# Kernel optimization log

Measured on AMD Instinct MI355X. Metric: run time of the kernel, lower is better.

Reference implementation:

```python
import jax, jax.numpy as jnp
import numpy as np

N = 100000       # nodes
E = 3200000      # edges (avg degree 32)
IN = 64          # in_channels
HID = 32         # hidden_channels
HEADS = 2
OUT = 1
EPS = 1e-5       # LayerNorm eps
SLOPE = 0.2      # LeakyReLU negative slope (PyG default)


def setup_inputs() -> dict:
    key = jax.random.key(0)
    ks = jax.random.split(key, 18)
    def nrm(k, shape, scale=0.1):
        return jax.random.normal(k, shape, dtype=jnp.float32) * scale
    return {
        "x": jax.random.normal(ks[0], (N, IN), dtype=jnp.float32),
        "edge_index": jax.random.randint(ks[1], (2, E), 0, N, dtype=jnp.int64),
        # GATConv layer 1 (concat=True)
        "W1": nrm(ks[2], (IN, HEADS * HID)),
        "a_src1": nrm(ks[3], (HEADS, HID)),
        "a_dst1": nrm(ks[4], (HEADS, HID)),
        "b1": jnp.zeros((HEADS * HID,), jnp.float32),
        "ln1_g": jnp.ones((HEADS * HID,), jnp.float32),
        "ln1_b": jnp.zeros((HEADS * HID,), jnp.float32),
        # GATConv layer 2 (heads=1, concat=False)
        "W2": nrm(ks[5], (HEADS * HID, HID)),
        "a_src2": nrm(ks[6], (1, HID)),
        "a_dst2": nrm(ks[7], (1, HID)),
        "b2": jnp.zeros((HID,), jnp.float32),
        "ln2_g": jnp.ones((HID,), jnp.float32),
        "ln2_b": jnp.zeros((HID,), jnp.float32),
        # output Linear
        "Wout": nrm(ks[8], (HID, OUT)),
        "bout": jnp.zeros((OUT,), jnp.float32),
    }


def layer_norm(x, g, b):
    mu = jnp.mean(x, axis=-1, keepdims=True)
    var = jnp.mean(jnp.square(x - mu), axis=-1, keepdims=True)
    return (x - mu) * jax.lax.rsqrt(var + EPS) * g + b


def gat_conv(x, edge_index, W, a_src, a_dst, bias, heads, ch, concat):
    """PyG GATConv (add_self_loops=True, bias=True), eval mode (no dropout)."""
    n = x.shape[0]
    loop = jnp.arange(n, dtype=edge_index.dtype)
    src = jnp.concatenate([edge_index[0], loop])   # [E+N]
    dst = jnp.concatenate([edge_index[1], loop])   # [E+N]
    h = (x @ W).reshape(n, heads, ch)              # [N,H,C]
    al_src = jnp.sum(h * a_src, axis=-1)           # [N,H]
    al_dst = jnp.sum(h * a_dst, axis=-1)           # [N,H]
    logits = jax.nn.leaky_relu(al_src[src] + al_dst[dst], SLOPE)  # [E+N,H]
    # segment softmax over destination nodes
    m = jax.lax.stop_gradient(jax.ops.segment_max(logits, dst, num_segments=n))
    e = jnp.exp(logits - m[dst])
    denom = jax.ops.segment_sum(e, dst, num_segments=n)
    alpha = e / denom[dst]                         # [E+N,H]
    out = jax.ops.segment_sum(h[src] * alpha[:, :, None], dst, num_segments=n)  # [N,H,C]
    out = out.reshape(n, heads * ch) if concat else out.mean(axis=1)
    return out + bias


def reference(x, edge_index, W1, a_src1, a_dst1, b1, ln1_g, ln1_b,
              W2, a_src2, a_dst2, b2, ln2_g, ln2_b, Wout, bout):
    h = gat_conv(x, edge_index, W1, a_src1, a_dst1, b1, HEADS, HID, True)
    h = jax.nn.elu(layer_norm(h, ln1_g, ln1_b))
    h = gat_conv(h, edge_index, W2, a_src2, a_dst2, b2, 1, HID, False)
    h = jax.nn.elu(layer_norm(h, ln2_g, ln2_b))
    return h @ Wout + bout  # [N, OUT]
```

## Files before the change

### kernel.cpp

```cpp
#include <hip/hip_runtime.h>

#define EPS 1e-5f
#define SLOPE 0.2f
#define MAXK 512
#define SEGCAP 12288
#define PBATCH 8192

__device__ __forceinline__ float leaky(float z) {
    return fmaxf(z, 0.f) + SLOPE * fminf(z, 0.f);
}
__device__ __forceinline__ ushort f2bf(float f) {
    unsigned u = __float_as_uint(f);
    u += 0x7FFFu + ((u >> 16) & 1u);
    return (ushort)(u >> 16);
}
__device__ __forceinline__ float bf2f(ushort b) {
    return __uint_as_float(((unsigned)b) << 16);
}

__global__ __launch_bounds__(1024) void part1(
    const int* __restrict__ ei, int E, int K, int* __restrict__ segcnt,
    unsigned* __restrict__ part) {
    __shared__ int h[MAXK];
    __shared__ int gp[MAXK];
    __shared__ int run[MAXK];
    int t = threadIdx.x;
    for (int i = t; i < K; i += 1024) { h[i] = 0; run[i] = 0; }
    __syncthreads();
    int base = blockIdx.x * PBATCH;
    int sv[PBATCH / 1024], dv[PBATCH / 1024];
#pragma unroll
    for (int j = 0; j < PBATCH / 1024; j++) {
        int e = base + j * 1024 + t;
        sv[j] = (e < E) ? ei[e] : -1;
        dv[j] = (e < E) ? ei[E + e] : -1;
        if (dv[j] >= 0) atomicAdd(&h[dv[j] >> 8], 1);
    }
    __syncthreads();
    for (int i = t; i < K; i += 1024)
        gp[i] = h[i] ? atomicAdd(&segcnt[i * 16], h[i]) : 0;
    __syncthreads();
#pragma unroll
    for (int j = 0; j < PBATCH / 1024; j++) {
        if (dv[j] >= 0) {
            int b = dv[j] >> 8;
            int p = atomicAdd(&run[b], 1) + gp[b];
            if (p < SEGCAP)
                part[(size_t)b * SEGCAP + p] =
                    ((unsigned)sv[j] << 8) | (unsigned)(dv[j] & 255);
        }
    }
}

__global__ __launch_bounds__(256) void sortseg(
    const int* __restrict__ segcnt, int N,
    unsigned* __restrict__ part, int* __restrict__ nodeofs, int* __restrict__ cnt,
    int* __restrict__ perm) {
    __shared__ int h2[4096];
    __shared__ int sc[256];
    __shared__ int ex[256];
    __shared__ unsigned outb[SEGCAP];
    int b = blockIdx.x, t = threadIdx.x;
    size_t base = (size_t)b * SEGCAP;
    int sz = min(segcnt[b * 16], SEGCAP);
    for (int i = t; i < 4096; i += 256) h2[i] = 0;
    __syncthreads();
    for (int i = t; i < sz; i += 256) {
        unsigned code = part[base + i];
        int key = ((code & 255) << 4) | ((code >> 21) & 15);
        atomicAdd(&h2[key], 1);
    }
    __syncthreads();
    int loc[16];
    int v = 0;
#pragma unroll
    for (int i = 0; i < 16; i++) { loc[i] = h2[t * 16 + i]; v += loc[i]; }
    sc[t] = v;
    __syncthreads();
    for (int off = 1; off < 256; off <<= 1) {
        int x = (t >= off) ? sc[t - off] : 0;
        __syncthreads();
        sc[t] += x;
        __syncthreads();
    }
    int exv = sc[t] - v;
    {
        int run = exv;
#pragma unroll
        for (int i = 0; i < 16; i++) { h2[t * 16 + i] = run; run += loc[i]; }
    }
    int n = b * 256 + t;
    if (n < N) { cnt[n] = v; nodeofs[n] = (int)(base + exv); }
    __syncthreads();
    for (int i = t; i < sz; i += 256) {
        unsigned code = part[base + i];
        int key = ((code & 255) << 4) | ((code >> 21) & 15);
        int p = atomicAdd(&h2[key], 1);
        outb[p] = code >> 8;
    }
    __syncthreads();
    for (int i = t; i < sz; i += 256) part[base + i] = outb[i];
    __syncthreads();
    h2[t] = 0;
    __syncthreads();
    int dbin = min(v, 255);
    if (n < N) atomicAdd(&h2[dbin], 1);
    __syncthreads();
    int hv = h2[t];
    sc[t] = hv;
    __syncthreads();
    for (int off = 1; off < 256; off <<= 1) {
        int x = (t >= off) ? sc[t - off] : 0;
        __syncthreads();
        sc[t] += x;
        __syncthreads();
    }
    ex[t] = sc[t] - hv;
    __syncthreads();
    if (n < N) {
        int r = atomicAdd(&ex[dbin], 1);
        perm[b * 256 + r] = n;
    }
}

__global__ __launch_bounds__(256) void prep1(
    const float* __restrict__ x, const float* __restrict__ W1,
    const float* __restrict__ as1, const float* __restrict__ ad1,
    ushort* __restrict__ h1b, float* __restrict__ al_s, float* __restrict__ al_d, int N) {
    __shared__ float Ws[64 * 64];
    __shared__ float xs[16][68];
    int t = threadIdx.x;
    for (int i = t; i < 64 * 64; i += 256) Ws[i] = W1[i];
    int base = blockIdx.x * 16;
    for (int i = t; i < 256; i += 256) {
        int rr = i >> 4, kk = i & 15;
        int gr = base + rr;
        float4 vx = (gr < N) ? ((const float4*)x)[(size_t)gr * 16 + kk]
                             : make_float4(0.f, 0.f, 0.f, 0.f);
        *(float4*)&xs[rr][kk * 4] = vx;
    }
    __syncthreads();
    int wv = t >> 6, c = t & 63;
    int r0 = base + wv * 4;
    float acc0 = 0.f, acc1 = 0.f, acc2 = 0.f, acc3 = 0.f;
#pragma unroll
    for (int k = 0; k < 64; k += 4) {
        float4 x0 = *(const float4*)&xs[wv * 4 + 0][k];
        float4 x1 = *(const float4*)&xs[wv * 4 + 1][k];
        float4 x2 = *(const float4*)&xs[wv * 4 + 2][k];
        float4 x3 = *(const float4*)&xs[wv * 4 + 3][k];
        float w0 = Ws[(k + 0) * 64 + c];
        float w1 = Ws[(k + 1) * 64 + c];
        float w2 = Ws[(k + 2) * 64 + c];
        float w3 = Ws[(k + 3) * 64 + c];
        acc0 = fmaf(x0.x, w0, acc0); acc1 = fmaf(x1.x, w0, acc1);
        acc2 = fmaf(x2.x, w0, acc2); acc3 = fmaf(x3.x, w0, acc3);
        acc0 = fmaf(x0.y, w1, acc0); acc1 = fmaf(x1.y, w1, acc1);
        acc2 = fmaf(x2.y, w1, acc2); acc3 = fmaf(x3.y, w1, acc3);
        acc0 = fmaf(x0.z, w2, acc0); acc1 = fmaf(x1.z, w2, acc1);
        acc2 = fmaf(x2.z, w2, acc2); acc3 = fmaf(x3.z, w2, acc3);
        acc0 = fmaf(x0.w, w3, acc0); acc1 = fmaf(x1.w, w3, acc1);
        acc2 = fmaf(x2.w, w3, acc2); acc3 = fmaf(x3.w, w3, acc3);
    }
    int head = c >> 5, cc = c & 31;
    float asc = as1[head * 32 + cc], adc = ad1[head * 32 + cc];
    float vs0 = acc0 * asc, vd0 = acc0 * adc;
    float vs1 = acc1 * asc, vd1 = acc1 * adc;
    float vs2 = acc2 * asc, vd2 = acc2 * adc;
    float vs3 = acc3 * asc, vd3 = acc3 * adc;
#pragma unroll
    for (int off = 1; off < 32; off <<= 1) {
        vs0 += __shfl_xor(vs0, off); vd0 += __shfl_xor(vd0, off);
        vs1 += __shfl_xor(vs1, off); vd1 += __shfl_xor(vd1, off);
        vs2 += __shfl_xor(vs2, off); vd2 += __shfl_xor(vd2, off);
        vs3 += __shfl_xor(vs3, off); vd3 += __shfl_xor(vd3, off);
    }
    if (r0 + 0 < N) h1b[(size_t)(r0 + 0) * 64 + c] = f2bf(acc0);
    if (r0 + 1 < N) h1b[(size_t)(r0 + 1) * 64 + c] = f2bf(acc1);
    if (r0 + 2 < N) h1b[(size_t)(r0 + 2) * 64 + c] = f2bf(acc2);
    if (r0 + 3 < N) h1b[(size_t)(r0 + 3) * 64 + c] = f2bf(acc3);
    if (cc == 0) {
        if (r0 + 0 < N) { al_s[(r0 + 0) * 2 + head] = vs0; al_d[(r0 + 0) * 2 + head] = vd0; }
        if (r0 + 1 < N) { al_s[(r0 + 1) * 2 + head] = vs1; al_d[(r0 + 1) * 2 + head] = vd1; }
        if (r0 + 2 < N) { al_s[(r0 + 2) * 2 + head] = vs2; al_d[(r0 + 2) * 2 + head] = vd2; }
        if (r0 + 3 < N) { al_s[(r0 + 3) * 2 + head] = vs3; al_d[(r0 + 3) * 2 + head] = vd3; }
    }
}

__global__ __launch_bounds__(256) void aggB1(
    const ushort* __restrict__ h1b, const float* __restrict__ als,
    const float* __restrict__ ald, const int* __restrict__ nodeofs,
    const int* __restrict__ cnt, const unsigned* __restrict__ csr,
    const int* __restrict__ perm,
    const float* __restrict__ b1, const float* __restrict__ g1,
    const float* __restrict__ bb1, ushort* __restrict__ h1out, int N) {
    int lane = threadIdx.x & 63;
    int grp = lane >> 4, q = lane & 15;
    int gbase = grp << 4;
    int idx = blockIdx.x * 16 + (threadIdx.x >> 6) * 4 + grp;
    bool valid = idx < N;
    int nc = perm[min(idx, N - 1)];
    int head = q >> 3;
    const float2* als2 = (const float2*)als;
    const float2* ald2 = (const float2*)ald;
    float2 adv = ald2[nc], asv = als2[nc];
    float ad0 = adv.x, ad1v = adv.y;
    float wsf = __expf(leaky((head ? asv.y : asv.x) + (head ? ad1v : ad0)));
    const ushort4* h4 = (const ushort4*)h1b;
    ushort4 hs = h4[(unsigned)nc * 16 + q];
    float a0 = wsf * bf2f(hs.x), a1 = wsf * bf2f(hs.y);
    float a2 = wsf * bf2f(hs.z), a3 = wsf * bf2f(hs.w);
    float l0p = 0.f, l1p = 0.f;
    int ofs = valid ? nodeofs[nc] : 0;
    int deg = valid ? cnt[nc] : 0;
    int degm1 = max(deg - 1, 0);
    int degmax = deg;
    degmax = max(degmax, __shfl_xor(degmax, 16));
    degmax = max(degmax, __shfl_xor(degmax, 32));
    for (int eb = 0; eb < degmax; eb += 16) {
        int j = ofs + min(eb + q, degm1);
        int sq = min((int)csr[j], N - 1);
        float2 av = als2[sq];
        float z0 = leaky(av.x + ad0);
        float z1 = leaky(av.y + ad1v);
        bool ev = (eb + q < deg);
        float w0q = ev ? __expf(z0) : 0.f;
        float w1q = ev ? __expf(z1) : 0.f;
        l0p += w0q;
        l1p += w1q;
#pragma unroll
        for (int jj = 0; jj < 16; jj++) {
            int s = __shfl(sq, gbase + jj);
            float w0 = __shfl(w0q, gbase + jj);
            float w1 = __shfl(w1q, gbase + jj);
            float w = head ? w1 : w0;
            ushort4 hv = h4[(unsigned)s * 16 + q];
            a0 = fmaf(w, bf2f(hv.x), a0);
            a1 = fmaf(w, bf2f(hv.y), a1);
            a2 = fmaf(w, bf2f(hv.z), a2);
            a3 = fmaf(w, bf2f(hv.w), a3);
        }
    }
#pragma unroll
    for (int off = 1; off < 16; off <<= 1) {
        l0p += __shfl_xor(l0p, off);
        l1p += __shfl_xor(l1p, off);
    }
    if (!valid) return;
    float l = (head ? l1p : l0p) + wsf;
    float inv = 1.f / l;
    float4 bv = ((const float4*)b1)[q];
    float v0 = a0 * inv + bv.x, v1 = a1 * inv + bv.y;
    float v2 = a2 * inv + bv.z, v3 = a3 * inv + bv.w;
    float s1 = v0 + v1 + v2 + v3;
#pragma unroll
    for (int off = 1; off < 16; off <<= 1) s1 += __shfl_xor(s1, off);
    float mu = s1 * (1.f / 64.f);
    float d0 = v0 - mu, d1 = v1 - mu, d2 = v2 - mu, d3 = v3 - mu;
    float s2v = d0 * d0 + d1 * d1 + d2 * d2 + d3 * d3;
#pragma unroll
    for (int off = 1; off < 16; off <<= 1) s2v += __shfl_xor(s2v, off);
    float rs = rsqrtf(s2v * (1.f / 64.f) + EPS);
    float4 gv = ((const float4*)g1)[q];
    float4 bbv = ((const float4*)bb1)[q];
    float y0 = d0 * rs * gv.x + bbv.x;
    float y1 = d1 * rs * gv.y + bbv.y;
    float y2 = d2 * rs * gv.z + bbv.z;
    float y3 = d3 * rs * gv.w + bbv.w;
    y0 = (y0 > 0.f) ? y0 : (__expf(y0) - 1.f);
    y1 = (y1 > 0.f) ? y1 : (__expf(y1) - 1.f);
    y2 = (y2 > 0.f) ? y2 : (__expf(y2) - 1.f);
    y3 = (y3 > 0.f) ? y3 : (__expf(y3) - 1.f);
    ((ushort4*)h1out)[(unsigned)nc * 16 + q] =
        make_ushort4(f2bf(y0), f2bf(y1), f2bf(y2), f2bf(y3));
}

__global__ __launch_bounds__(256) void prep2(
    const ushort* __restrict__ h1ob, const float* __restrict__ W2,
    const float* __restrict__ as2, const float* __restrict__ ad2,
    ushort* __restrict__ h2b, float* __restrict__ al_s, float* __restrict__ al_d, int N) {
    __shared__ float Ws[64 * 32];
    __shared__ float xs[32][68];
    int t = threadIdx.x;
    for (int i = t; i < 64 * 32; i += 256) Ws[i] = W2[i];
    int base = blockIdx.x * 32;
    const ushort4* hv4 = (const ushort4*)h1ob;
    for (int i = t; i < 512; i += 256) {
        int rr = i >> 4, kk = i & 15;
        int gr = base + rr;
        ushort4 u = (gr < N) ? hv4[(unsigned)gr * 16 + kk] : make_ushort4(0, 0, 0, 0);
        xs[rr][kk * 4 + 0] = bf2f(u.x);
        xs[rr][kk * 4 + 1] = bf2f(u.y);
        xs[rr][kk * 4 + 2] = bf2f(u.z);
        xs[rr][kk * 4 + 3] = bf2f(u.w);
    }
    __syncthreads();
    int wv = t >> 6;
    int lane = t & 63;
    int half = lane >> 5, c = lane & 31;
    int rbase = wv * 8 + half * 4;
    int r0 = base + rbase;
    float acc0 = 0.f, acc1 = 0.f, acc2 = 0.f, acc3 = 0.f;
#pragma unroll
    for (int k = 0; k < 64; k += 4) {
        float4 x0 = *(const float4*)&xs[rbase + 0][k];
        float4 x1 = *(const float4*)&xs[rbase + 1][k];
        float4 x2 = *(const float4*)&xs[rbase + 2][k];
        float4 x3 = *(const float4*)&xs[rbase + 3][k];
        float w0 = Ws[(k + 0) * 32 + c];
        float w1 = Ws[(k + 1) * 32 + c];
        float w2 = Ws[(k + 2) * 32 + c];
        float w3 = Ws[(k + 3) * 32 + c];
        acc0 = fmaf(x0.x, w0, acc0); acc1 = fmaf(x1.x, w0, acc1);
        acc2 = fmaf(x2.x, w0, acc2); acc3 = fmaf(x3.x, w0, acc3);
        acc0 = fmaf(x0.y, w1, acc0); acc1 = fmaf(x1.y, w1, acc1);
        acc2 = fmaf(x2.y, w1, acc2); acc3 = fmaf(x3.y, w1, acc3);
        acc0 = fmaf(x0.z, w2, acc0); acc1 = fmaf(x1.z, w2, acc1);
        acc2 = fmaf(x2.z, w2, acc2); acc3 = fmaf(x3.z, w2, acc3);
        acc0 = fmaf(x0.w, w3, acc0); acc1 = fmaf(x1.w, w3, acc1);
        acc2 = fmaf(x2.w, w3, acc2); acc3 = fmaf(x3.w, w3, acc3);
    }
    float asc = as2[c], adc = ad2[c];
    float vs0 = acc0 * asc, vd0 = acc0 * adc;
    float vs1 = acc1 * asc, vd1 = acc1 * adc;
    float vs2 = acc2 * asc, vd2 = acc2 * adc;
    float vs3 = acc3 * asc, vd3 = acc3 * adc;
#pragma unroll
    for (int off = 1; off < 32; off <<= 1) {
        vs0 += __shfl_xor(vs0, off); vd0 += __shfl_xor(vd0, off);
        vs1 += __shfl_xor(vs1, off); vd1 += __shfl_xor(vd1, off);
        vs2 += __shfl_xor(vs2, off); vd2 += __shfl_xor(vd2, off);
        vs3 += __shfl_xor(vs3, off); vd3 += __shfl_xor(vd3, off);
    }
    if (r0 + 0 < N) h2b[(size_t)(r0 + 0) * 32 + c] = f2bf(acc0);
    if (r0 + 1 < N) h2b[(size_t)(r0 + 1) * 32 + c] = f2bf(acc1);
    if (r0 + 2 < N) h2b[(size_t)(r0 + 2) * 32 + c] = f2bf(acc2);
    if (r0 + 3 < N) h2b[(size_t)(r0 + 3) * 32 + c] = f2bf(acc3);
    if (c == 0) {
        if (r0 + 0 < N) { al_s[r0 + 0] = vs0; al_d[r0 + 0] = vd0; }
        if (r0 + 1 < N) { al_s[r0 + 1] = vs1; al_d[r0 + 1] = vd1; }
        if (r0 + 2 < N) { al_s[r0 + 2] = vs2; al_d[r0 + 2] = vd2; }
        if (r0 + 3 < N) { al_s[r0 + 3] = vs3; al_d[r0 + 3] = vd3; }
    }
}

__global__ __launch_bounds__(256) void aggB2(
    const ushort* __restrict__ h2b, const float* __restrict__ als,
    const float* __restrict__ ald, const int* __restrict__ nodeofs,
    const int* __restrict__ cnt, const unsigned* __restrict__ csr,
    const int* __restrict__ perm,
    const float* __restrict__ b2, const float* __restrict__ g2,
    const float* __restrict__ bb2, const float* __restrict__ Wout,
    const float* __restrict__ bout, float* __restrict__ out, int N) {
    int lane = threadIdx.x & 63;
    int grp = lane >> 3, q = lane & 7;
    int gbase = grp << 3;
    int idx = blockIdx.x * 32 + (threadIdx.x >> 6) * 8 + grp;
    bool valid = idx < N;
    int nc = perm[min(idx, N - 1)];
    float myad = ald[nc];
    float wsf = __expf(leaky(als[nc] + myad));
    const ushort4* h4 = (const ushort4*)h2b;
    ushort4 hs = h4[(unsigned)nc * 8 + q];
    float a0 = wsf * bf2f(hs.x), a1 = wsf * bf2f(hs.y);
    float a2 = wsf * bf2f(hs.z), a3 = wsf * bf2f(hs.w);
    float lp = 0.f;
    int ofs = valid ? nodeofs[nc] : 0;
    int deg = valid ? cnt[nc] : 0;
    int degm1 = max(deg - 1, 0);
    int degmax = deg;
    degmax = max(degmax, __shfl_xor(degmax, 8));
    degmax = max(degmax, __shfl_xor(degmax, 16));
    degmax = max(degmax, __shfl_xor(degmax, 32));
    for (int eb = 0; eb < degmax; eb += 8) {
        int j = ofs + min(eb + q, degm1);
        int sq = min((int)csr[j], N - 1);
        float z = leaky(als[sq] + myad);
        float wq = (eb + q < deg) ? __expf(z) : 0.f;
        lp += wq;
#pragma unroll
        for (int jj = 0; jj < 8; jj++) {
            int s = __shfl(sq, gbase + jj);
            float w = __shfl(wq, gbase + jj);
            ushort4 hv = h4[(unsigned)s * 8 + q];
            a0 = fmaf(w, bf2f(hv.x), a0);
            a1 = fmaf(w, bf2f(hv.y), a1);
            a2 = fmaf(w, bf2f(hv.z), a2);
            a3 = fmaf(w, bf2f(hv.w), a3);
        }
    }
#pragma unroll
    for (int off = 1; off < 8; off <<= 1) lp += __shfl_xor(lp, off);
    if (!valid) return;
    float l = lp + wsf;
    float inv = 1.f / l;
    float4 bv = ((const float4*)b2)[q];
    float v0 = a0 * inv + bv.x, v1 = a1 * inv + bv.y;
    float v2 = a2 * inv + bv.z, v3 = a3 * inv + bv.w;
    float s1 = v0 + v1 + v2 + v3;
#pragma unroll
    for (int off = 1; off < 8; off <<= 1) s1 += __shfl_xor(s1, off);
    float mu = s1 * (1.f / 32.f);
    float d0 = v0 - mu, d1 = v1 - mu, d2 = v2 - mu, d3 = v3 - mu;
    float s2v = d0 * d0 + d1 * d1 + d2 * d2 + d3 * d3;
#pragma unroll
    for (int off = 1; off < 8; off <<= 1) s2v += __shfl_xor(s2v, off);
    float rs = rsqrtf(s2v * (1.f / 32.f) + EPS);
    float4 gv = ((const float4*)g2)[q];
    float4 bbv = ((const float4*)bb2)[q];
    float y0 = d0 * rs * gv.x + bbv.x;
    float y1 = d1 * rs * gv.y + bbv.y;
    float y2 = d2 * rs * gv.z + bbv.z;
    float y3 = d3 * rs * gv.w + bbv.w;
    y0 = (y0 > 0.f) ? y0 : (__expf(y0) - 1.f);
    y1 = (y1 > 0.f) ? y1 : (__expf(y1) - 1.f);
    y2 = (y2 > 0.f) ? y2 : (__expf(y2) - 1.f);
    y3 = (y3 > 0.f) ? y3 : (__expf(y3) - 1.f);
    float4 wo = ((const float4*)Wout)[q];
    float p = y0 * wo.x + y1 * wo.y + y2 * wo.z + y3 * wo.w;
#pragma unroll
    for (int off = 1; off < 8; off <<= 1) p += __shfl_xor(p, off);
    if (q == 0) out[nc] = p + bout[0];
}

extern "C" void kernel_launch(void* const* d_in, const int* in_sizes, int n_in,
                              void* d_out, int out_size, void* d_ws, size_t ws_size,
                              hipStream_t stream) {
    const float* x    = (const float*)d_in[0];
    const int*   ei   = (const int*)d_in[1];
    const float* W1   = (const float*)d_in[2];
    const float* as1  = (const float*)d_in[3];
    const float* ad1  = (const float*)d_in[4];
    const float* b1   = (const float*)d_in[5];
    const float* g1   = (const float*)d_in[6];
    const float* bb1  = (const float*)d_in[7];
    const float* W2   = (const float*)d_in[8];
    const float* as2  = (const float*)d_in[9];
    const float* ad2  = (const float*)d_in[10];
    const float* b2   = (const float*)d_in[11];
    const float* g2   = (const float*)d_in[12];
    const float* bb2  = (const float*)d_in[13];
    const float* Wout = (const float*)d_in[14];
    const float* bout = (const float*)d_in[15];
    float* out = (float*)d_out;

    const int N = in_sizes[0] / 64;
    const int E = in_sizes[1] / 2;
    const int K = (N + 255) / 256;

    auto align_up = [](size_t v) { return (v + 255) & ~(size_t)255; };
    char* ws = (char*)d_ws;
    unsigned* part    = (unsigned*)ws; ws += align_up((size_t)K * SEGCAP * 4);
    int*      segcnt  = (int*)ws;      ws += align_up((size_t)MAXK * 16 * 4);
    int*      nodeofs = (int*)ws;      ws += align_up((size_t)N * 4);
    int*      cnt     = (int*)ws;      ws += align_up((size_t)N * 4);
    int*      perm    = (int*)ws;      ws += align_up((size_t)(K * 256) * 4);
    ushort*   h1b     = (ushort*)ws;   ws += align_up((size_t)N * 64 * 2);
    ushort*   h1ob    = (ushort*)ws;   ws += align_up((size_t)N * 64 * 2);
    ushort*   h2b     = (ushort*)ws;   ws += align_up((size_t)N * 32 * 2);
    float*    al1s    = (float*)ws;    ws += align_up((size_t)N * 2 * 4);
    float*    al1d    = (float*)ws;    ws += align_up((size_t)N * 2 * 4);
    float*    al2s    = (float*)ws;    ws += align_up((size_t)N * 4);
    float*    al2d    = (float*)ws;    ws += align_up((size_t)N * 4);

    const int EB = (E + PBATCH - 1) / PBATCH;

    hipMemsetAsync(segcnt, 0, (size_t)K * 16 * 4, stream);
    part1<<<EB, 1024, 0, stream>>>(ei, E, K, segcnt, part);
    sortseg<<<K, 256, 0, stream>>>(segcnt, N, part, nodeofs, cnt, perm);

    prep1<<<(N + 15) / 16, 256, 0, stream>>>(x, W1, as1, ad1, h1b, al1s, al1d, N);
    aggB1<<<(N + 15) / 16, 256, 0, stream>>>(h1b, al1s, al1d, nodeofs, cnt, part,
                                             perm, b1, g1, bb1, h1ob, N);
    prep2<<<(N + 31) / 32, 256, 0, stream>>>(h1ob, W2, as2, ad2, h2b, al2s, al2d, N);
    aggB2<<<(N + 31) / 32, 256, 0, stream>>>(h2b, al2s, al2d, nodeofs, cnt, part,
                                             perm, b2, g2, bb2, Wout, bout, out, N);
}
```

Before: 327.8 us.

## Fuse edge partition with layer-1 projection and layer-2 projection into aggregation

Merges the edge-partitioning kernel and the first linear projection into one launch, with block index selecting the role, so the projection runs alongside partitioning. Moves the second layer's linear projection and attention-logit computation into the first aggregation kernel using warp shuffles and W2 in shared memory. This removes the intermediate bf16 layer-1 output buffer round trip and two kernel launches. In exchange, the fused kernels use more shared memory and registers, and the 1024-thread projection blocks may lower occupancy.

Measured after the change: 319.8 us. 1.02x faster.

```diff
diff --git a/kernel.cpp b/kernel.cpp
--- a/kernel.cpp
+++ b/kernel.cpp
@@ -18,122 +18,52 @@
     return __uint_as_float(((unsigned)b) << 16);
 }
 
-__global__ __launch_bounds__(1024) void part1(
+__global__ __launch_bounds__(1024) void fused1(
     const int* __restrict__ ei, int E, int K, int* __restrict__ segcnt,
-    unsigned* __restrict__ part) {
-    __shared__ int h[MAXK];
-    __shared__ int gp[MAXK];
-    __shared__ int run[MAXK];
-    int t = threadIdx.x;
-    for (int i = t; i < K; i += 1024) { h[i] = 0; run[i] = 0; }
-    __syncthreads();
-    int base = blockIdx.x * PBATCH;
-    int sv[PBATCH / 1024], dv[PBATCH / 1024];
-#pragma unroll
-    for (int j = 0; j < PBATCH / 1024; j++) {
-        int e = base + j * 1024 + t;
-        sv[j] = (e < E) ? ei[e] : -1;
-        dv[j] = (e < E) ? ei[E + e] : -1;
-        if (dv[j] >= 0) atomicAdd(&h[dv[j] >> 8], 1);
-    }
-    __syncthreads();
-    for (int i = t; i < K; i += 1024)
-        gp[i] = h[i] ? atomicAdd(&segcnt[i * 16], h[i]) : 0;
-    __syncthreads();
-#pragma unroll
-    for (int j = 0; j < PBATCH / 1024; j++) {
-        if (dv[j] >= 0) {
-            int b = dv[j] >> 8;
-            int p = atomicAdd(&run[b], 1) + gp[b];
-            if (p < SEGCAP)
-                part[(size_t)b * SEGCAP + p] =
-                    ((unsigned)sv[j] << 8) | (unsigned)(dv[j] & 255);
-        }
-    }
-}
-
-__global__ __launch_bounds__(256) void sortseg(
-    const int* __restrict__ segcnt, int N,
-    unsigned* __restrict__ part, int* __restrict__ nodeofs, int* __restrict__ cnt,
-    int* __restrict__ perm) {
-    __shared__ int h2[4096];
-    __shared__ int sc[256];
-    __shared__ int ex[256];
-    __shared__ unsigned outb[SEGCAP];
-    int b = blockIdx.x, t = threadIdx.x;
-    size_t base = (size_t)b * SEGCAP;
-    int sz = min(segcnt[b * 16], SEGCAP);
-    for (int i = t; i < 4096; i += 256) h2[i] = 0;
-    __syncthreads();
-    for (int i = t; i < sz; i += 256) {
-        unsigned code = part[base + i];
-        int key = ((code & 255) << 4) | ((code >> 21) & 15);
-        atomicAdd(&h2[key], 1);
-    }
-    __syncthreads();
-    int loc[16];
-    int v = 0;
-#pragma unroll
-    for (int i = 0; i < 16; i++) { loc[i] = h2[t * 16 + i]; v += loc[i]; }
-    sc[t] = v;
-    __syncthreads();
-    for (int off = 1; off < 256; off <<= 1) {
-        int x = (t >= off) ? sc[t - off] : 0;
-        __syncthreads();
-        sc[t] += x;
-        __syncthreads();
-    }
-    int exv = sc[t] - v;
-    {
-        int run = exv;
-#pragma unroll
-        for (int i = 0; i < 16; i++) { h2[t * 16 + i] = run; run += loc[i]; }
-    }
-    int n = b * 256 + t;
-    if (n < N) { cnt[n] = v; nodeofs[n] = (int)(base + exv); }
-    __syncthreads();
-    for (int i = t; i < sz; i += 256) {
-        unsigned code = part[base + i];
-        int key = ((code & 255) << 4) | ((code >> 21) & 15);
-        int p = atomicAdd(&h2[key], 1);
-        outb[p] = code >> 8;
-    }
-    __syncthreads();
-    for (int i = t; i < sz; i += 256) part[base + i] = outb[i];
-    __syncthreads();
-    h2[t] = 0;
-    __syncthreads();
-    int dbin = min(v, 255);
-    if (n < N) atomicAdd(&h2[dbin], 1);
-    __syncthreads();
-    int hv = h2[t];
-    sc[t] = hv;
-    __syncthreads();
-    for (int off = 1; off < 256; off <<= 1) {
-        int x = (t >= off) ? sc[t - off] : 0;
-        __syncthreads();
-        sc[t] += x;
-        __syncthreads();
-    }
-    ex[t] = sc[t] - hv;
-    __syncthreads();
-    if (n < N) {
-        int r = atomicAdd(&ex[dbin], 1);
-        perm[b * 256 + r] = n;
-    }
-}
-
-__global__ __launch_bounds__(256) void prep1(
+    unsigned* __restrict__ part,
     const float* __restrict__ x, const float* __restrict__ W1,
     const float* __restrict__ as1, const float* __restrict__ ad1,
-    ushort* __restrict__ h1b, float* __restrict__ al_s, float* __restrict__ al_d, int N) {
-    __shared__ float Ws[64 * 64];
-    __shared__ float xs[16][68];
+    ushort* __restrict__ h1b, float* __restrict__ al_s, float* __restrict__ al_d,
+    int N, int EB) {
+    __shared__ float smem[4096 + 64 * 68];
     int t = threadIdx.x;
-    for (int i = t; i < 64 * 64; i += 256) Ws[i] = W1[i];
-    int base = blockIdx.x * 16;
-    for (int i = t; i < 256; i += 256) {
-        int rr = i >> 4, kk = i & 15;
+    if ((int)blockIdx.x < EB) {
+        int* h   = (int*)smem;
+        int* gp  = h + 512;
+        int* run = h + 1024;
+        for (int i = t; i < K; i += 1024) { h[i] = 0; run[i] = 0; }
+        __syncthreads();
+        int base = blockIdx.x * PBATCH;
+        int sv[PBATCH / 1024], dv[PBATCH / 1024];
+#pragma unroll
+        for (int j = 0; j < PBATCH / 1024; j++) {
+            int e = base + j * 1024 + t;
+            sv[j] = (e < E) ? ei[e] : -1;
+            dv[j] = (e < E) ? ei[E + e] : -1;
+            if (dv[j] >= 0) atomicAdd(&h[dv[j] >> 8], 1);
+        }
+        __syncthreads();
+        for (int i = t; i < K; i += 1024)
+            gp[i] = h[i] ? atomicAdd(&segcnt[i * 16], h[i]) : 0;
+        __syncthreads();
+#pragma unroll
+        for (int j = 0; j < PBATCH / 1024; j++) {
+            if (dv[j] >= 0) {
+                int b = dv[j] >> 8;
+                int p = atomicAdd(&run[b], 1) + gp[b];
+                if (p < SEGCAP)
+                    part[(size_t)b * SEGCAP + p] =
+                        ((unsigned)sv[j] << 8) | (unsigned)(dv[j] & 255);
+            }
+        }
+        return;
+    }
+    float* Ws = smem;
+    float (*xs)[68] = (float(*)[68])(smem + 4096);
+    for (int i = t; i < 4096; i += 1024) Ws[i] = W1[i];
+    int base = (blockIdx.x - EB) * 64;
+    {
+        int rr = t >> 4, kk = t & 15;
         int gr = base + rr;
         float4 vx = (gr < N) ? ((const float4*)x)[(size_t)gr * 16 + kk]
                              : make_float4(0.f, 0.f, 0.f, 0.f);
@@ -187,17 +117,96 @@
     }
 }
 
+__global__ __launch_bounds__(256) void sortseg(
+    const int* __restrict__ segcnt, int N,
+    unsigned* __restrict__ part, int* __restrict__ nodeofs, int* __restrict__ cnt,
+    int* __restrict__ perm) {
+    __shared__ int h2[4096];
+    __shared__ int sc[256];
+    __shared__ int ex[256];
+    __shared__ unsigned outb[SEGCAP];
+    int b = blockIdx.x, t = threadIdx.x;
+    size_t base = (size_t)b * SEGCAP;
+    int sz = min(segcnt[b * 16], SEGCAP);
+    for (int i = t; i < 4096; i += 256) h2[i] = 0;
+    __syncthreads();
+    for (int i = t; i < sz; i += 256) {
+        unsigned code = part[base + i];
+        int key = ((code & 255) << 4) | ((code >> 21) & 15);
+        atomicAdd(&h2[key], 1);
+    }
+    __syncthreads();
+    int loc[16];
+    int v = 0;
+#pragma unroll
+    for (int i = 0; i < 16; i++) { loc[i] = h2[t * 16 + i]; v += loc[i]; }
+    sc[t] = v;
+    __syncthreads();
+    for (int off = 1; off < 256; off <<= 1) {
+        int x = (t >= off) ? sc[t - off] : 0;
+        __syncthreads();
+        sc[t] += x;
+        __syncthreads();
+    }
+    int exv = sc[t] - v;
+    {
+        int run = exv;
+#pragma unroll
+        for (int i = 0; i < 16; i++) { h2[t * 16 + i] = run; run += loc[i]; }
+    }
+    int n = b * 256 + t;
+    if (n < N) { cnt[n] = v; nodeofs[n] = (int)(base + exv); }
+    __syncthreads();
+    for (int i = t; i < sz; i += 256) {
+        unsigned code = part[base + i];
+        int key = ((code & 255) << 4) | ((code >> 21) & 15);
+        int p = atomicAdd(&h2[key], 1);
+        outb[p] = code >> 8;
+    }
+    __syncthreads();
+    for (int i = t; i < sz; i += 256) part[base + i] = outb[i];
+    __syncthreads();
+    h2[t] = 0;
+    __syncthreads();
+    int dbin = min(v, 255);
+    if (n < N) atomicAdd(&h2[dbin], 1);
+    __syncthreads();
+    int hv = h2[t];
+    sc[t] = hv;
+    __syncthreads();
+    for (int off = 1; off < 256; off <<= 1) {
+        int x = (t >= off) ? sc[t - off] : 0;
+        __syncthreads();
+        sc[t] += x;
+        __syncthreads();
+    }
+    ex[t] = sc[t] - hv;
+    __syncthreads();
+    if (n < N) {
+        int r = atomicAdd(&ex[dbin], 1);
+        perm[b * 256 + r] = n;
+    }
+}
+
 __global__ __launch_bounds__(256) void aggB1(
     const ushort* __restrict__ h1b, const float* __restrict__ als,
     const float* __restrict__ ald, const int* __restrict__ nodeofs,
     const int* __restrict__ cnt, const unsigned* __restrict__ csr,
     const int* __restrict__ perm,
     const float* __restrict__ b1, const float* __restrict__ g1,
-    const float* __restrict__ bb1, ushort* __restrict__ h1out, int N) {
-    int lane = threadIdx.x & 63;
+    const float* __restrict__ bb1,
+    const float* __restrict__ W2, const float* __restrict__ as2,
+    const float* __restrict__ ad2,
+    ushort* __restrict__ h2b, float* __restrict__ al2s, float* __restrict__ al2d,
+    int N) {
+    __shared__ float W2s[64 * 32];
+    int t = threadIdx.x;
+    for (int i = t; i < 2048; i += 256) W2s[i] = W2[i];
+    __syncthreads();
+    int lane = t & 63;
     int grp = lane >> 4, q = lane & 15;
     int gbase = grp << 4;
-    int idx = blockIdx.x * 16 + (threadIdx.x >> 6) * 4 + grp;
+    int idx = blockIdx.x * 16 + (t >> 6) * 4 + grp;
     bool valid = idx < N;
     int nc = perm[min(idx, N - 1)];
     int head = q >> 3;
@@ -271,77 +280,36 @@
     y1 = (y1 > 0.f) ? y1 : (__expf(y1) - 1.f);
     y2 = (y2 > 0.f) ? y2 : (__expf(y2) - 1.f);
     y3 = (y3 > 0.f) ? y3 : (__expf(y3) - 1.f);
-    ((ushort4*)h1out)[(unsigned)nc * 16 + q] =
-        make_ushort4(f2bf(y0), f2bf(y1), f2bf(y2), f2bf(y3));
-}
-
-__global__ __launch_bounds__(256) void prep2(
-    const ushort* __restrict__ h1ob, const float* __restrict__ W2,
-    const float* __restrict__ as2, const float* __restrict__ ad2,
-    ushort* __restrict__ h2b, float* __restrict__ al_s, float* __restrict__ al_d, int N) {
-    __shared__ float Ws[64 * 32];
-    __shared__ float xs[32][68];
-    int t = threadIdx.x;
-    for (int i = t; i < 64 * 32; i += 256) Ws[i] = W2[i];
-    int base = blockIdx.x * 32;
-    const ushort4* hv4 = (const ushort4*)h1ob;
-    for (int i = t; i < 512; i += 256) {
-        int rr = i >> 4, kk = i & 15;
-        int gr = base + rr;
-        ushort4 u = (gr < N) ? hv4[(unsigned)gr * 16 + kk] : make_ushort4(0, 0, 0, 0);
-        xs[rr][kk * 4 + 0] = bf2f(u.x);
-        xs[rr][kk * 4 + 1] = bf2f(u.y);
-        xs[rr][kk * 4 + 2] = bf2f(u.z);
-        xs[rr][kk * 4 + 3] = bf2f(u.w);
-    }
-    __syncthreads();
-    int wv = t >> 6;
-    int lane = t & 63;
-    int half = lane >> 5, c = lane & 31;
-    int rbase = wv * 8 + half * 4;
-    int r0 = base + rbase;
-    float acc0 = 0.f, acc1 = 0.f, acc2 = 0.f, acc3 = 0.f;
-#pragma unroll
-    for (int k = 0; k < 64; k += 4) {
-        float4 x0 = *(const float4*)&xs[rbase + 0][k];
-        float4 x1 = *(const float4*)&xs[rbase + 1][k];
-        float4 x2 = *(const float4*)&xs[rbase + 2][k];
-        float4 x3 = *(const float4*)&xs[rbase + 3][k];
-        float w0 = Ws[(k + 0) * 32 + c];
-        float w1 = Ws[(k + 1) * 32 + c];
-        float w2 = Ws[(k + 2) * 32 + c];
-        float w3 = Ws[(k + 3) * 32 + c];
-        acc0 = fmaf(x0.x, w0, acc0); acc1 = fmaf(x1.x, w0, acc1);
-        acc2 = fmaf(x2.x, w0, acc2); acc3 = fmaf(x3.x, w0, acc3);
-        acc0 = fmaf(x0.y, w1, acc0); acc1 = fmaf(x1.y, w1, acc1);
-        acc2 = fmaf(x2.y, w1, acc2); acc3 = fmaf(x3.y, w1, acc3);
-        acc0 = fmaf(x0.z, w2, acc0); acc1 = fmaf(x1.z, w2, acc1);
-        acc2 = fmaf(x2.z, w2, acc2); acc3 = fmaf(x3.z, w2, acc3);
-        acc0 = fmaf(x0.w, w3, acc0); acc1 = fmaf(x1.w, w3, acc1);
-        acc2 = fmaf(x2.w, w3, acc2); acc3 = fmaf(x3.w, w3, acc3);
-    }
-    float asc = as2[c], adc = ad2[c];
-    float vs0 = acc0 * asc, vd0 = acc0 * adc;
-    float vs1 = acc1 * asc, vd1 = acc1 * adc;
-    float vs2 = acc2 * asc, vd2 = acc2 * adc;
-    float vs3 = acc3 * asc, vd3 = acc3 * adc;
-#pragma unroll
-    for (int off = 1; off < 32; off <<= 1) {
-        vs0 += __shfl_xor(vs0, off); vd0 += __shfl_xor(vd0, off);
-        vs1 += __shfl_xor(vs1, off); vd1 += __shfl_xor(vd1, off);
-        vs2 += __shfl_xor(vs2, off); vd2 += __shfl_xor(vd2, off);
-        vs3 += __shfl_xor(vs3, off); vd3 += __shfl_xor(vd3, off);
-    }
-    if (r0 + 0 < N) h2b[(size_t)(r0 + 0) * 32 + c] = f2bf(acc0);
-    if (r0 + 1 < N) h2b[(size_t)(r0 + 1) * 32 + c] = f2bf(acc1);
-    if (r0 + 2 < N) h2b[(size_t)(r0 + 2) * 32 + c] = f2bf(acc2);
-    if (r0 + 3 < N) h2b[(size_t)(r0 + 3) * 32 + c] = f2bf(acc3);
-    if (c == 0) {
-        if (r0 + 0 < N) { al_s[r0 + 0] = vs0; al_d[r0 + 0] = vd0; }
-        if (r0 + 1 < N) { al_s[r0 + 1] = vs1; al_d[r0 + 1] = vd1; }
-        if (r0 + 2 < N) { al_s[r0 + 2] = vs2; al_d[r0 + 2] = vd2; }
-        if (r0 + 3 < N) { al_s[r0 + 3] = vs3; al_d[r0 + 3] = vd3; }
-    }
+    float hacc0 = 0.f, hacc1 = 0.f;
+    int c0 = q * 2;
+#pragma unroll
+    for (int jj = 0; jj < 16; jj++) {
+        float t0 = __shfl(y0, gbase + jj);
+        float t1 = __shfl(y1, gbase + jj);
+        float t2 = __shfl(y2, gbase + jj);
+        float t3 = __shfl(y3, gbase + jj);
+        int k = jj * 4;
+        hacc0 = fmaf(t0, W2s[(k + 0) * 32 + c0], hacc0);
+        hacc1 = fmaf(t0, W2s[(k + 0) * 32 + c0 + 1], hacc1);
+        hacc0 = fmaf(t1, W2s[(k + 1) * 32 + c0], hacc0);
+        hacc1 = fmaf(t1, W2s[(k + 1) * 32 + c0 + 1], hacc1);
+        hacc0 = fmaf(t2, W2s[(k + 2) * 32 + c0], hacc0);
+        hacc1 = fmaf(t2, W2s[(k + 2) * 32 + c0 + 1], hacc1);
+        hacc0 = fmaf(t3, W2s[(k + 3) * 32 + c0], hacc0);
+        hacc1 = fmaf(t3, W2s[(k + 3) * 32 + c0 + 1], hacc1);
+    }
+    ushort2 hw;
+    hw.x = f2bf(hacc0);
+    hw.y = f2bf(hacc1);
+    ((ushort2*)h2b)[(unsigned)nc * 16 + q] = hw;
+    float vs = hacc0 * as2[c0] + hacc1 * as2[c0 + 1];
+    float vd = hacc0 * ad2[c0] + hacc1 * ad2[c0 + 1];
+#pragma unroll
+    for (int off = 1; off < 16; off <<= 1) {
+        vs += __shfl_xor(vs, off);
+        vd += __shfl_xor(vd, off);
+    }
+    if (q == 0) { al2s[nc] = vs; al2d[nc] = vd; }
 }
 
 __global__ __launch_bounds__(256) void aggB2(
@@ -456,7 +424,6 @@
     int*      cnt     = (int*)ws;      ws += align_up((size_t)N * 4);
     int*      perm    = (int*)ws;      ws += align_up((size_t)(K * 256) * 4);
     ushort*   h1b     = (ushort*)ws;   ws += align_up((size_t)N * 64 * 2);
-    ushort*   h1ob    = (ushort*)ws;   ws += align_up((size_t)N * 64 * 2);
     ushort*   h2b     = (ushort*)ws;   ws += align_up((size_t)N * 32 * 2);
     float*    al1s    = (float*)ws;    ws += align_up((size_t)N * 2 * 4);
     float*    al1d    = (float*)ws;    ws += align_up((size_t)N * 2 * 4);
@@ -464,15 +431,15 @@
     float*    al2d    = (float*)ws;    ws += align_up((size_t)N * 4);
 
     const int EB = (E + PBATCH - 1) / PBATCH;
+    const int PB = (N + 63) / 64;
 
     hipMemsetAsync(segcnt, 0, (size_t)K * 16 * 4, stream);
-    part1<<<EB, 1024, 0, stream>>>(ei, E, K, segcnt, part);
+    fused1<<<EB + PB, 1024, 0, stream>>>(ei, E, K, segcnt, part,
+                                         x, W1, as1, ad1, h1b, al1s, al1d, N, EB);
     sortseg<<<K, 256, 0, stream>>>(segcnt, N, part, nodeofs, cnt, perm);
-
-    prep1<<<(N + 15) / 16, 256, 0, stream>>>(x, W1, as1, ad1, h1b, al1s, al1d, N);
     aggB1<<<(N + 15) / 16, 256, 0, stream>>>(h1b, al1s, al1d, nodeofs, cnt, part,
-                                             perm, b1, g1, bb1, h1ob, N);
-    prep2<<<(N + 31) / 32, 256, 0, stream>>>(h1ob, W2, as2, ad2, h2b, al2s, al2d, N);
+                                             perm, b1, g1, bb1,
+                                             W2, as2, ad2, h2b, al2s, al2d, N);
     aggB2<<<(N + 31) / 32, 256, 0, stream>>>(h2b, al2s, al2d, nodeofs, cnt, part,
                                              perm, b2, g2, bb2, Wout, bout, out, N);
 }
```

## Fuse edge partitioning and layer-1 projection into one heterogeneous kernel launch

Applied to the files above, without the earlier changes.

Merges the edge bucketing kernel and the first-layer feature projection (x@W1 plus attention logits) into a single launch. Block ID picks the role: the first EB blocks partition edges, the rest run the projection with 1024 threads over 64 rows each. The two independent stages can now run concurrently and one launch is dropped. The cost is larger shared memory and 1024-thread blocks for the projection, which may lower occupancy.

Measured after the change: 320.4 us. 2.3% less time.

```diff
diff --git a/kernel.cpp b/kernel.cpp
--- a/kernel.cpp
+++ b/kernel.cpp
@@ -18,122 +18,52 @@
     return __uint_as_float(((unsigned)b) << 16);
 }
 
-__global__ __launch_bounds__(1024) void part1(
+__global__ __launch_bounds__(1024) void fused1(
     const int* __restrict__ ei, int E, int K, int* __restrict__ segcnt,
-    unsigned* __restrict__ part) {
-    __shared__ int h[MAXK];
-    __shared__ int gp[MAXK];
-    __shared__ int run[MAXK];
-    int t = threadIdx.x;
-    for (int i = t; i < K; i += 1024) { h[i] = 0; run[i] = 0; }
-    __syncthreads();
-    int base = blockIdx.x * PBATCH;
-    int sv[PBATCH / 1024], dv[PBATCH / 1024];
-#pragma unroll
-    for (int j = 0; j < PBATCH / 1024; j++) {
-        int e = base + j * 1024 + t;
-        sv[j] = (e < E) ? ei[e] : -1;
-        dv[j] = (e < E) ? ei[E + e] : -1;
-        if (dv[j] >= 0) atomicAdd(&h[dv[j] >> 8], 1);
-    }
-    __syncthreads();
-    for (int i = t; i < K; i += 1024)
-        gp[i] = h[i] ? atomicAdd(&segcnt[i * 16], h[i]) : 0;
-    __syncthreads();
-#pragma unroll
-    for (int j = 0; j < PBATCH / 1024; j++) {
-        if (dv[j] >= 0) {
-            int b = dv[j] >> 8;
-            int p = atomicAdd(&run[b], 1) + gp[b];
-            if (p < SEGCAP)
-                part[(size_t)b * SEGCAP + p] =
-                    ((unsigned)sv[j] << 8) | (unsigned)(dv[j] & 255);
-        }
-    }
-}
-
-__global__ __launch_bounds__(256) void sortseg(
-    const int* __restrict__ segcnt, int N,
-    unsigned* __restrict__ part, int* __restrict__ nodeofs, int* __restrict__ cnt,
-    int* __restrict__ perm) {
-    __shared__ int h2[4096];
-    __shared__ int sc[256];
-    __shared__ int ex[256];
-    __shared__ unsigned outb[SEGCAP];
-    int b = blockIdx.x, t = threadIdx.x;
-    size_t base = (size_t)b * SEGCAP;
-    int sz = min(segcnt[b * 16], SEGCAP);
-    for (int i = t; i < 4096; i += 256) h2[i] = 0;
-    __syncthreads();
-    for (int i = t; i < sz; i += 256) {
-        unsigned code = part[base + i];
-        int key = ((code & 255) << 4) | ((code >> 21) & 15);
-        atomicAdd(&h2[key], 1);
-    }
-    __syncthreads();
-    int loc[16];
-    int v = 0;
-#pragma unroll
-    for (int i = 0; i < 16; i++) { loc[i] = h2[t * 16 + i]; v += loc[i]; }
-    sc[t] = v;
-    __syncthreads();
-    for (int off = 1; off < 256; off <<= 1) {
-        int x = (t >= off) ? sc[t - off] : 0;
-        __syncthreads();
-        sc[t] += x;
-        __syncthreads();
-    }
-    int exv = sc[t] - v;
-    {
-        int run = exv;
-#pragma unroll
-        for (int i = 0; i < 16; i++) { h2[t * 16 + i] = run; run += loc[i]; }
-    }
-    int n = b * 256 + t;
-    if (n < N) { cnt[n] = v; nodeofs[n] = (int)(base + exv); }
-    __syncthreads();
-    for (int i = t; i < sz; i += 256) {
-        unsigned code = part[base + i];
-        int key = ((code & 255) << 4) | ((code >> 21) & 15);
-        int p = atomicAdd(&h2[key], 1);
-        outb[p] = code >> 8;
-    }
-    __syncthreads();
-    for (int i = t; i < sz; i += 256) part[base + i] = outb[i];
-    __syncthreads();
-    h2[t] = 0;
-    __syncthreads();
-    int dbin = min(v, 255);
-    if (n < N) atomicAdd(&h2[dbin], 1);
-    __syncthreads();
-    int hv = h2[t];
-    sc[t] = hv;
-    __syncthreads();
-    for (int off = 1; off < 256; off <<= 1) {
-        int x = (t >= off) ? sc[t - off] : 0;
-        __syncthreads();
-        sc[t] += x;
-        __syncthreads();
-    }
-    ex[t] = sc[t] - hv;
-    __syncthreads();
-    if (n < N) {
-        int r = atomicAdd(&ex[dbin], 1);
-        perm[b * 256 + r] = n;
-    }
-}
-
-__global__ __launch_bounds__(256) void prep1(
+    unsigned* __restrict__ part,
     const float* __restrict__ x, const float* __restrict__ W1,
     const float* __restrict__ as1, const float* __restrict__ ad1,
-    ushort* __restrict__ h1b, float* __restrict__ al_s, float* __restrict__ al_d, int N) {
-    __shared__ float Ws[64 * 64];
-    __shared__ float xs[16][68];
+    ushort* __restrict__ h1b, float* __restrict__ al_s, float* __restrict__ al_d,
+    int N, int EB) {
+    __shared__ float smem[4096 + 64 * 68];
     int t = threadIdx.x;
-    for (int i = t; i < 64 * 64; i += 256) Ws[i] = W1[i];
-    int base = blockIdx.x * 16;
-    for (int i = t; i < 256; i += 256) {
-        int rr = i >> 4, kk = i & 15;
+    if ((int)blockIdx.x < EB) {
+        int* h   = (int*)smem;
+        int* gp  = h + 512;
+        int* run = h + 1024;
+        for (int i = t; i < K; i += 1024) { h[i] = 0; run[i] = 0; }
+        __syncthreads();
+        int base = blockIdx.x * PBATCH;
+        int sv[PBATCH / 1024], dv[PBATCH / 1024];
+#pragma unroll
+        for (int j = 0; j < PBATCH / 1024; j++) {
+            int e = base + j * 1024 + t;
+            sv[j] = (e < E) ? ei[e] : -1;
+            dv[j] = (e < E) ? ei[E + e] : -1;
+            if (dv[j] >= 0) atomicAdd(&h[dv[j] >> 8], 1);
+        }
+        __syncthreads();
+        for (int i = t; i < K; i += 1024)
+            gp[i] = h[i] ? atomicAdd(&segcnt[i * 16], h[i]) : 0;
+        __syncthreads();
+#pragma unroll
+        for (int j = 0; j < PBATCH / 1024; j++) {
+            if (dv[j] >= 0) {
+                int b = dv[j] >> 8;
+                int p = atomicAdd(&run[b], 1) + gp[b];
+                if (p < SEGCAP)
+                    part[(size_t)b * SEGCAP + p] =
+                        ((unsigned)sv[j] << 8) | (unsigned)(dv[j] & 255);
+            }
+        }
+        return;
+    }
+    float* Ws = smem;
+    float (*xs)[68] = (float(*)[68])(smem + 4096);
+    for (int i = t; i < 4096; i += 1024) Ws[i] = W1[i];
+    int base = (blockIdx.x - EB) * 64;
+    {
+        int rr = t >> 4, kk = t & 15;
         int gr = base + rr;
         float4 vx = (gr < N) ? ((const float4*)x)[(size_t)gr * 16 + kk]
                              : make_float4(0.f, 0.f, 0.f, 0.f);
@@ -184,6 +114,77 @@
         if (r0 + 1 < N) { al_s[(r0 + 1) * 2 + head] = vs1; al_d[(r0 + 1) * 2 + head] = vd1; }
         if (r0 + 2 < N) { al_s[(r0 + 2) * 2 + head] = vs2; al_d[(r0 + 2) * 2 + head] = vd2; }
         if (r0 + 3 < N) { al_s[(r0 + 3) * 2 + head] = vs3; al_d[(r0 + 3) * 2 + head] = vd3; }
+    }
+}
+
+__global__ __launch_bounds__(256) void sortseg(
+    const int* __restrict__ segcnt, int N,
+    unsigned* __restrict__ part, int* __restrict__ nodeofs, int* __restrict__ cnt,
+    int* __restrict__ perm) {
+    __shared__ int h2[4096];
+    __shared__ int sc[256];
+    __shared__ int ex[256];
+    __shared__ unsigned outb[SEGCAP];
+    int b = blockIdx.x, t = threadIdx.x;
+    size_t base = (size_t)b * SEGCAP;
+    int sz = min(segcnt[b * 16], SEGCAP);
+    for (int i = t; i < 4096; i += 256) h2[i] = 0;
+    __syncthreads();
+    for (int i = t; i < sz; i += 256) {
+        unsigned code = part[base + i];
+        int key = ((code & 255) << 4) | ((code >> 21) & 15);
+        atomicAdd(&h2[key], 1);
+    }
+    __syncthreads();
+    int loc[16];
+    int v = 0;
+#pragma unroll
+    for (int i = 0; i < 16; i++) { loc[i] = h2[t * 16 + i]; v += loc[i]; }
+    sc[t] = v;
+    __syncthreads();
+    for (int off = 1; off < 256; off <<= 1) {
+        int x = (t >= off) ? sc[t - off] : 0;
+        __syncthreads();
+        sc[t] += x;
+        __syncthreads();
+    }
+    int exv = sc[t] - v;
+    {
+        int run = exv;
+#pragma unroll
+        for (int i = 0; i < 16; i++) { h2[t * 16 + i] = run; run += loc[i]; }
+    }
+    int n = b * 256 + t;
+    if (n < N) { cnt[n] = v; nodeofs[n] = (int)(base + exv); }
+    __syncthreads();
+    for (int i = t; i < sz; i += 256) {
+        unsigned code = part[base + i];
+        int key = ((code & 255) << 4) | ((code >> 21) & 15);
+        int p = atomicAdd(&h2[key], 1);
+        outb[p] = code >> 8;
+    }
+    __syncthreads();
+    for (int i = t; i < sz; i += 256) part[base + i] = outb[i];
+    __syncthreads();
+    h2[t] = 0;
+    __syncthreads();
+    int dbin = min(v, 255);
+    if (n < N) atomicAdd(&h2[dbin], 1);
+    __syncthreads();
+    int hv = h2[t];
+    sc[t] = hv;
+    __syncthreads();
+    for (int off = 1; off < 256; off <<= 1) {
+        int x = (t >= off) ? sc[t - off] : 0;
+        __syncthreads();
+        sc[t] += x;
+        __syncthreads();
+    }
+    ex[t] = sc[t] - hv;
+    __syncthreads();
+    if (n < N) {
+        int r = atomicAdd(&ex[dbin], 1);
+        perm[b * 256 + r] = n;
     }
 }
 
@@ -464,12 +465,12 @@
     float*    al2d    = (float*)ws;    ws += align_up((size_t)N * 4);
 
     const int EB = (E + PBATCH - 1) / PBATCH;
+    const int PB = (N + 63) / 64;
 
     hipMemsetAsync(segcnt, 0, (size_t)K * 16 * 4, stream);
-    part1<<<EB, 1024, 0, stream>>>(ei, E, K, segcnt, part);
+    fused1<<<EB + PB, 1024, 0, stream>>>(ei, E, K, segcnt, part,
+                                         x, W1, as1, ad1, h1b, al1s, al1d, N, EB);
     sortseg<<<K, 256, 0, stream>>>(segcnt, N, part, nodeofs, cnt, perm);
-
-    prep1<<<(N + 15) / 16, 256, 0, stream>>>(x, W1, as1, ad1, h1b, al1s, al1d, N);
     aggB1<<<(N + 15) / 16, 256, 0, stream>>>(h1b, al1s, al1d, nodeofs, cnt, part,
                                              perm, b1, g1, bb1, h1ob, N);
     prep2<<<(N + 31) / 32, 256, 0, stream>>>(h1ob, W2, as2, ad2, h2b, al2s, al2d, N);
```
